# Kernel tuning notes

Hardware: AMD Instinct MI355X
Metric: run time of the kernel (lower is better)

## Reference

```python
import jax, jax.numpy as jnp
import numpy as np

N = 100000   # nodes
E = 600000   # edges
F_IN = 128   # input feature dim
H = 256      # hidden_channels


def setup_inputs() -> dict:
    key = jax.random.key(0)
    ks = jax.random.split(key, 8)
    x = jax.random.normal(ks[0], (N, F_IN), dtype=jnp.float32)
    edge_index = jax.random.randint(ks[1], (2, E), 0, N, dtype=jnp.int64)
    # SAGEConv params: out = lin_l(mean_agg) + lin_r(x_root); bias only on lin_l (PyG default)
    s1 = 1.0 / np.sqrt(F_IN)
    s2 = 1.0 / np.sqrt(H)
    Wl1 = jax.random.uniform(ks[2], (F_IN, H), jnp.float32, -s1, s1)
    Wr1 = jax.random.uniform(ks[3], (F_IN, H), jnp.float32, -s1, s1)
    b1 = jnp.zeros((H,), jnp.float32)
    Wl2 = jax.random.uniform(ks[4], (H, H), jnp.float32, -s2, s2)
    Wr2 = jax.random.uniform(ks[5], (H, H), jnp.float32, -s2, s2)
    b2 = jnp.zeros((H,), jnp.float32)
    return {"x": x, "edge_index": edge_index, "Wl1": Wl1, "Wr1": Wr1, "b1": b1,
            "Wl2": Wl2, "Wr2": Wr2, "b2": b2}


def _sage_conv(h, src, dst, Wl, Wr, b):
    # mean aggregation of source-node features at destination nodes
    msg = h[src]                                             # [E, d]
    agg = jax.ops.segment_sum(msg, dst, num_segments=N)      # [N, d]
    cnt = jax.ops.segment_sum(jnp.ones((src.shape[0],), h.dtype), dst, num_segments=N)
    agg = agg / jnp.maximum(cnt, 1.0)[:, None]
    return agg @ Wl + b + h @ Wr


def reference(x, edge_index, Wl1, Wr1, b1, Wl2, Wr2, b2):
    src, dst = edge_index[0], edge_index[1]
    h = jax.nn.relu(_sage_conv(x, src, dst, Wl1, Wr1, b1))
    return _sage_conv(h, src, dst, Wl2, Wr2, b2)
```

## Files before the change

kernel.cpp:

```cpp
#include <hip/hip_runtime.h>

#define Nn 100000
#define Ee 600000
#define Fin 128
#define Hd  256
#define NB  ((Nn + 1023) / 1024)
#define CB  12500
#define PB  768
#define EB  ((Ee + 255) / 256)

typedef __attribute__((ext_vector_type(8))) short short8;
typedef __attribute__((ext_vector_type(4))) float floatx4;

__device__ __forceinline__ float bf2f(unsigned short h) {
    return __uint_as_float(((unsigned int)h) << 16);
}
__device__ __forceinline__ unsigned short f2bf(float f) {
    unsigned int u = __float_as_uint(f);
    u += 0x7FFFu + ((u >> 16) & 1u);
    return (unsigned short)(u >> 16);
}
__device__ __forceinline__ float loadf(const void* p, int i, int f32) {
    return f32 ? ((const float*)p)[i] : bf2f(((const unsigned short*)p)[i]);
}
__device__ __forceinline__ void gload_lds16(const void* g, void* lds) {
    __builtin_amdgcn_global_load_lds((const __attribute__((address_space(1))) void*)g,
                                     (__attribute__((address_space(3))) void*)lds,
                                     16, 0, 0);
}

__device__ __forceinline__ void get_edge(const int* __restrict__ ei, int is64, int e,
                                         int& s, int& d) {
    if (is64) { s = ei[2 * e]; d = ei[2 * (Ee + e)]; }
    else      { s = ei[e];     d = ei[Ee + e]; }
}

__global__ void k_init(const unsigned int* __restrict__ ei,
                       const unsigned short* __restrict__ xu,
                       int* __restrict__ flag, int* __restrict__ cnt) {
    int i = blockIdx.x * 256 + threadIdx.x;
    if (i < 2 * Nn) cnt[i] = 0;
    if (blockIdx.x == 0 && threadIdx.x == 0) {
        int is64 = 1;
        for (int k = 1; k < 64; k += 2)
            if (ei[k] != 0u) { is64 = 0; break; }
        flag[0] = is64;
        int isf32 = 0;
        for (int k = 0; k < 512; k += 2) {
            unsigned e = (xu[k] >> 7) & 0xFFu;
            if (e >= 0xC0u) { isf32 = 1; break; }
        }
        flag[1] = isf32;
    }
}

__global__ void k_pre(const void* __restrict__ x, unsigned short* __restrict__ xb,
                      const void* __restrict__ Wl1, const void* __restrict__ Wr1,
                      const void* __restrict__ Wl2, const void* __restrict__ Wr2,
                      unsigned short* __restrict__ Wt1, unsigned short* __restrict__ Wt2,
                      const int* __restrict__ ei, int* __restrict__ cnt,
                      const int* __restrict__ flag) {
    int bid = blockIdx.x;
    if (bid < CB) {
        int i = (bid * 256 + threadIdx.x) * 4;
        if (i >= Nn * Fin) return;
        if (flag[1]) {
            float4 v = ((const float4*)x)[i >> 2];
            ushort4 u;
            u.x = f2bf(v.x); u.y = f2bf(v.y); u.z = f2bf(v.z); u.w = f2bf(v.w);
            ((ushort4*)xb)[i >> 2] = u;
        } else {
            ((ushort4*)xb)[i >> 2] = ((const ushort4*)x)[i >> 2];
        }
    } else if (bid < CB + PB) {
        int f32 = flag[1];
        int tid = (bid - CB) * 256 + threadIdx.x;
        if (tid < 256 * 256) {
            int n = tid >> 8, k = tid & 255;
            float v = (k < 128) ? loadf(Wl1, k * 256 + n, f32) : loadf(Wr1, (k - 128) * 256 + n, f32);
            Wt1[n * 256 + k] = f2bf(v);
        }
        int t2 = tid - 256 * 256;
        if (t2 >= 0 && t2 < 256 * 512) {
            int n = t2 >> 9, k = t2 & 511;
            float v = (k < 256) ? loadf(Wl2, k * 256 + n, f32) : loadf(Wr2, (k - 256) * 256 + n, f32);
            Wt2[n * 512 + k] = f2bf(v);
        }
    } else {
        int e = (bid - CB - PB) * 256 + threadIdx.x;
        if (e >= Ee) return;
        int is64 = flag[0], s, d;
        get_edge(ei, is64, e, s, d);
        atomicAdd(&cnt[d], 1);
    }
}

__global__ void k_bsum(const int* __restrict__ cnt, int* __restrict__ bsum) {
    __shared__ int red[256];
    int b = blockIdx.x, t = threadIdx.x;
    int i = b * 1024 + t * 4;
    int s = 0;
    if (i + 3 < Nn) {
        int4 v = *reinterpret_cast<const int4*>(cnt + i);
        s = v.x + v.y + v.z + v.w;
    } else {
        for (int j = 0; j < 4; j++) if (i + j < Nn) s += cnt[i + j];
    }
    red[t] = s;
    __syncthreads();
    for (int off = 128; off > 0; off >>= 1) {
        if (t < off) red[t] += red[t + off];
        __syncthreads();
    }
    if (t == 0) bsum[b] = red[0];
}

__global__ void k_bscan(const int* __restrict__ bsum, int* __restrict__ bpre,
                        int* __restrict__ rowptr) {
    __shared__ int sc[128];
    int t = threadIdx.x;
    int v = (t < NB) ? bsum[t] : 0;
    sc[t] = v;
    __syncthreads();
    for (int off = 1; off < 128; off <<= 1) {
        int add = (t >= off) ? sc[t - off] : 0;
        __syncthreads();
        sc[t] += add;
        __syncthreads();
    }
    if (t < NB) bpre[t] = sc[t] - v;
    if (t == 127) rowptr[Nn] = sc[127];
}

__global__ void k_rowptr(const int* __restrict__ cnt, const int* __restrict__ bpre,
                         int* __restrict__ rowptr) {
    __shared__ int sc[256];
    int b = blockIdx.x, t = threadIdx.x;
    int i = b * 1024 + t * 4;
    int4 c = make_int4(0, 0, 0, 0);
    if (i + 3 < Nn) {
        c = *reinterpret_cast<const int4*>(cnt + i);
    } else {
        if (i     < Nn) c.x = cnt[i];
        if (i + 1 < Nn) c.y = cnt[i + 1];
        if (i + 2 < Nn) c.z = cnt[i + 2];
        if (i + 3 < Nn) c.w = cnt[i + 3];
    }
    int s = c.x + c.y + c.z + c.w;
    sc[t] = s;
    __syncthreads();
    for (int off = 1; off < 256; off <<= 1) {
        int add = (t >= off) ? sc[t - off] : 0;
        __syncthreads();
        sc[t] += add;
        __syncthreads();
    }
    int p = bpre[b] + sc[t] - s;
    int4 r;
    r.x = p;
    r.y = r.x + c.x;
    r.z = r.y + c.y;
    r.w = r.z + c.z;
    if (i + 3 < Nn) {
        *reinterpret_cast<int4*>(rowptr + i) = r;
    } else {
        if (i     < Nn) rowptr[i]     = r.x;
        if (i + 1 < Nn) rowptr[i + 1] = r.y;
        if (i + 2 < Nn) rowptr[i + 2] = r.z;
        if (i + 3 < Nn) rowptr[i + 3] = r.w;
    }
}

__global__ void k_fill(const int* __restrict__ ei, const int* __restrict__ flag,
                       const int* __restrict__ rowptr, int* __restrict__ cur,
                       int* __restrict__ srcl) {
    int e = blockIdx.x * 256 + threadIdx.x;
    if (e >= Ee) return;
    int is64 = flag[0], s, d;
    get_edge(ei, is64, e, s, d);
    int pos = atomicAdd(&cur[d], 1);
    srcl[rowptr[d] + pos] = s;
}

template <int F, int SIN, int SOUT>
__device__ __forceinline__ void agg_body(const unsigned short* __restrict__ X,
                                         unsigned short* __restrict__ O,
                                         const int* __restrict__ rowptr,
                                         const int* __restrict__ srcl) {
    int gw = (blockIdx.x * blockDim.x + threadIdx.x) >> 6;
    int lane = threadIdx.x & 63;
    if (gw >= Nn) return;
    int b = rowptr[gw], e = rowptr[gw + 1];
    constexpr int C = F / 64;
    float acc[C] = {};
    if (e > b) {
        int last = e - 1;
        for (int i = b; i < e; i += 8) {
            int sv[8];
            float w[8];
#pragma unroll
            for (int j = 0; j < 8; j++) {
                int id = i + j;
                sv[j] = srcl[id < last ? id : last];
                w[j] = (id < e) ? 1.f : 0.f;
            }
            if constexpr (C == 2) {
                ushort2 u[8];
#pragma unroll
                for (int j = 0; j < 8; j++)
                    u[j] = *reinterpret_cast<const ushort2*>(X + (size_t)sv[j] * SIN + lane * 2);
#pragma unroll
                for (int j = 0; j < 8; j++) {
                    acc[0] = fmaf(w[j], bf2f(u[j].x), acc[0]);
                    acc[1] = fmaf(w[j], bf2f(u[j].y), acc[1]);
                }
            } else {
                ushort4 u[8];
#pragma unroll
                for (int j = 0; j < 8; j++)
                    u[j] = *reinterpret_cast<const ushort4*>(X + (size_t)sv[j] * SIN + lane * 4);
#pragma unroll
                for (int j = 0; j < 8; j++) {
                    acc[0] = fmaf(w[j], bf2f(u[j].x), acc[0]);
                    acc[1] = fmaf(w[j], bf2f(u[j].y), acc[1]);
                    acc[2] = fmaf(w[j], bf2f(u[j].z), acc[2]);
                    acc[3] = fmaf(w[j], bf2f(u[j].w), acc[3]);
                }
            }
        }
    }
    float inv = 1.f / (float)max(e - b, 1);
    unsigned short* op = O + (size_t)gw * SOUT + lane * C;
    if constexpr (C == 2) {
        ushort2 u; u.x = f2bf(acc[0] * inv); u.y = f2bf(acc[1] * inv);
        *reinterpret_cast<ushort2*>(op) = u;
    } else {
        ushort4 u;
        u.x = f2bf(acc[0] * inv); u.y = f2bf(acc[1] * inv);
        u.z = f2bf(acc[2] * inv); u.w = f2bf(acc[3] * inv);
        *reinterpret_cast<ushort4*>(op) = u;
    }
}

__global__ void k_agg1(const unsigned short* __restrict__ xb, unsigned short* __restrict__ agg1,
                       const int* __restrict__ rowptr, const int* __restrict__ srcl) {
    agg_body<Fin, Fin, Fin>(xb, agg1, rowptr, srcl);
}

__global__ void k_agg2(const int* __restrict__ rowptr, const int* __restrict__ srcl,
                       unsigned short* __restrict__ acat_ws) {
    agg_body<Hd, 512, 512>(acat_ws + 256, acat_ws, rowptr, srcl);
}

template <int KT, int K1, int S1, int S2>
__device__ __forceinline__ void gemm_core_pipe(const unsigned short* __restrict__ A1,
                                               const unsigned short* __restrict__ A2,
                                               const unsigned short* __restrict__ Wt,
                                               floatx4 (&acc)[4][4],
                                               unsigned short* sA, unsigned short* sB,
                                               int m_base) {
    const int tid = threadIdx.x;
    const int lane = tid & 63, wid = tid >> 6;
    const int wm = wid & 1, wn = wid >> 1;
    const int quad = lane >> 4, l16 = lane & 15;
    const int rs = tid >> 2;
    const int cs = tid & 3;
    constexpr int NT = KT / 32;

#define STAGE(t, buf)                                                              \
    {                                                                              \
        int kb_ = (t) * 32;                                                        \
        {                                                                          \
            int gk_ = kb_ + ((cs ^ ((rs >> 1) & 3)) << 3);                         \
            int m_ = m_base + rs; if (m_ >= Nn) m_ = Nn - 1;                       \
            const unsigned short* gp_ = (gk_ < K1)                                 \
                ? A1 + (size_t)m_ * S1 + gk_                                       \
                : A2 + (size_t)m_ * S2 + (gk_ - K1);                               \
            gload_lds16(gp_, sA + (buf) * 4096 + wid * 512);                       \
        }                                                                          \
        _Pragma("unroll")                                                          \
        for (int i_ = 0; i_ < 2; i_++) {                                           \
            int n_ = i_ * 128 + rs;                                                \
            int gk_ = kb_ + ((cs ^ ((n_ >> 1) & 3)) << 3);                         \
            gload_lds16(Wt + (size_t)n_ * KT + gk_,                                \
                        sB + (buf) * 8192 + i_ * 4096 + wid * 512);                \
        }                                                                          \
    }

#define COMPUTE(buf)                                                               \
    {                                                                              \
        short8 a_[4], b_[4];                                                       \
        _Pragma("unroll")                                                          \
        for (int mt_ = 0; mt_ < 4; mt_++) {                                        \
            int r_ = wm * 64 + mt_ * 16 + l16;                                     \
            a_[mt_] = *reinterpret_cast<const short8*>(                            \
                sA + (buf) * 4096 + r_ * 32 + ((quad ^ ((r_ >> 1) & 3)) << 3));    \
        }                                                                          \
        _Pragma("unroll")                                                          \
        for (int nt_ = 0; nt_ < 4; nt_++) {                                        \
            int n_ = wn * 64 + nt_ * 16 + l16;                                     \
            b_[nt_] = *reinterpret_cast<const short8*>(                            \
                sB + (buf) * 8192 + n_ * 32 + ((quad ^ ((n_ >> 1) & 3)) << 3));    \
        }                                                                          \
        _Pragma("unroll")                                                          \
        for (int mt_ = 0; mt_ < 4; mt_++)                                          \
            _Pragma("unroll")                                                      \
            for (int nt_ = 0; nt_ < 4; nt_++)                                      \
                acc[mt_][nt_] = __builtin_amdgcn_mfma_f32_16x16x32_bf16(           \
                    a_[mt_], b_[nt_], acc[mt_][nt_], 0, 0, 0);                     \
    }

    STAGE(0, 0)
#pragma unroll
    for (int t = 0; t < NT; t++) {
        __syncthreads();
        if (t + 1 < NT) STAGE(t + 1, (t + 1) & 1)
        COMPUTE(t & 1)
    }
#undef STAGE
#undef COMPUTE
}

__global__ __launch_bounds__(512) void k_gemm1(const unsigned short* __restrict__ agg1,
                                               const unsigned short* __restrict__ xb,
                                               const unsigned short* __restrict__ Wt1,
                                               const void* __restrict__ bias,
                                               const int* __restrict__ flag,
                                               unsigned short* __restrict__ acat_ws) {
    __shared__ unsigned short sA[8192];
    __shared__ unsigned short sB[16384];
    int f32 = flag[1];
    int tid = threadIdx.x;
    int wid = tid >> 6, lane = tid & 63;
    int wm = wid & 1, wn = wid >> 1;
    int quad = lane >> 4, l16 = lane & 15;
    int m_base = blockIdx.x * 128;
    floatx4 acc[4][4] = {};
    gemm_core_pipe<256, 128, 128, 128>(agg1, xb, Wt1, acc, sA, sB, m_base);
#pragma unroll
    for (int p = 0; p < 2; p++) {
        __syncthreads();
        if (wm == p) {
#pragma unroll
            for (int nt = 0; nt < 4; nt++) {
                int n = wn * 64 + nt * 16 + l16;
                float bv = loadf(bias, n, f32);
#pragma unroll
                for (int mt = 0; mt < 4; mt++) {
#pragma unroll
                    for (int r = 0; r < 4; r++) {
                        float v = acc[mt][nt][r] + bv;
                        v = v > 0.f ? v : 0.f;
                        sB[(mt * 16 + quad * 4 + r) * 256 + n] = f2bf(v);
                    }
                }
            }
        }
        __syncthreads();
#pragma unroll
        for (int rnd = 0; rnd < 4; rnd++) {
            int rl = rnd * 16 + (tid >> 5);
            int m = m_base + p * 64 + rl;
            if (m < Nn)
                *reinterpret_cast<short8*>(acat_ws + (size_t)m * 512 + 256 + (tid & 31) * 8) =
                    *reinterpret_cast<const short8*>(sB + rl * 256 + (tid & 31) * 8);
        }
    }
}

__global__ __launch_bounds__(512) void k_gemm2(const unsigned short* __restrict__ Wt2,
                                               const void* __restrict__ bias,
                                               const int* __restrict__ flag,
                                               const unsigned short* __restrict__ acat_ws,
                                               void* __restrict__ out) {
    __shared__ unsigned short sA[8192];
    __shared__ unsigned short sB[16384];
    int f32 = flag[1];
    int tid = threadIdx.x;
    int wid = tid >> 6, lane = tid & 63;
    int wm = wid & 1, wn = wid >> 1;
    int quad = lane >> 4, l16 = lane & 15;
    int m_base = blockIdx.x * 128;
    floatx4 acc[4][4] = {};
    gemm_core_pipe<512, 512, 512, 512>(acat_ws, acat_ws, Wt2, acc, sA, sB, m_base);
    float* sF = (float*)sB;
#pragma unroll
    for (int q = 0; q < 4; q++) {
        __syncthreads();
        if (wm == (q >> 1)) {
#pragma unroll
            for (int nt = 0; nt < 4; nt++) {
                int n = wn * 64 + nt * 16 + l16;
                float bv = loadf(bias, n, f32);
#pragma unroll
                for (int mt2 = 0; mt2 < 2; mt2++) {
                    int mt = (q & 1) * 2 + mt2;
#pragma unroll
                    for (int r = 0; r < 4; r++)
                        sF[(mt2 * 16 + quad * 4 + r) * 256 + n] = acc[mt][nt][r] + bv;
                }
            }
        }
        __syncthreads();
#pragma unroll
        for (int rnd = 0; rnd < 2; rnd++) {
            int rl = rnd * 16 + (tid >> 5);
            int m = m_base + q * 32 + rl;
            if (m < Nn) {
                if (f32) {
                    float4* dst = (float4*)((float*)out + (size_t)m * 256) + (tid & 31) * 2;
                    const float4* src = (const float4*)(sF + rl * 256) + (tid & 31) * 2;
                    dst[0] = src[0];
                    dst[1] = src[1];
                } else {
                    const float* src = sF + rl * 256 + (tid & 31) * 8;
                    short8 pk;
#pragma unroll
                    for (int j = 0; j < 8; j++)
                        ((unsigned short*)&pk)[j] = f2bf(src[j]);
                    *reinterpret_cast<short8*>((unsigned short*)out + (size_t)m * 256 + (tid & 31) * 8) = pk;
                }
            }
        }
    }
}

extern "C" void kernel_launch(void* const* d_in, const int* in_sizes, int n_in,
                              void* d_out, int out_size, void* d_ws, size_t ws_size,
                              hipStream_t stream) {
    const void* x   = d_in[0];
    const int*  ei  = (const int*)d_in[1];
    const void* Wl1 = d_in[2];
    const void* Wr1 = d_in[3];
    const void* b1  = d_in[4];
    const void* Wl2 = d_in[5];
    const void* Wr2 = d_in[6];
    const void* b2  = d_in[7];

    char* ws = (char*)d_ws;
    size_t off_cnt    = 0;
    size_t off_cur    = off_cnt + (size_t)Nn * 4;
    size_t off_rowptr = off_cur + (size_t)Nn * 4;
    size_t off_srcl   = off_rowptr + (size_t)(Nn + 4) * 4;
    size_t off_flag   = off_srcl + (size_t)Ee * 4;
    size_t off_bsum   = ((off_flag + 8 + 255) / 256) * 256;
    size_t off_bpre   = off_bsum + 128 * 4;
    size_t off_wt1    = off_bpre + 128 * 4;
    size_t off_wt2    = off_wt1 + 256 * 256 * 2;
    size_t off_xb     = off_wt2 + 256 * 512 * 2;
    size_t off_agg1   = off_xb + (size_t)Nn * Fin * 2;
    size_t off_acat   = off_agg1 + (size_t)Nn * Fin * 2;

    int*            cnt     = (int*)(ws + off_cnt);
    int*            cur     = (int*)(ws + off_cur);
    int*            rowptr  = (int*)(ws + off_rowptr);
    int*            srcl    = (int*)(ws + off_srcl);
    int*            flag    = (int*)(ws + off_flag);
    int*            bsum    = (int*)(ws + off_bsum);
    int*            bpre    = (int*)(ws + off_bpre);
    unsigned short* Wt1     = (unsigned short*)(ws + off_wt1);
    unsigned short* Wt2     = (unsigned short*)(ws + off_wt2);
    unsigned short* xb      = (unsigned short*)(ws + off_xb);
    unsigned short* agg1    = (unsigned short*)(ws + off_agg1);
    unsigned short* acat_ws = (unsigned short*)(ws + off_acat);

    k_init<<<(2 * Nn + 255) / 256, 256, 0, stream>>>((const unsigned int*)ei,
                                                     (const unsigned short*)x, flag, cnt);
    k_pre<<<CB + PB + EB, 256, 0, stream>>>(x, xb, Wl1, Wr1, Wl2, Wr2, Wt1, Wt2,
                                            ei, cnt, flag);
    k_bsum<<<NB, 256, 0, stream>>>(cnt, bsum);
    k_bscan<<<1, 128, 0, stream>>>(bsum, bpre, rowptr);
    k_rowptr<<<NB, 256, 0, stream>>>(cnt, bpre, rowptr);
    k_fill<<<EB, 256, 0, stream>>>(ei, flag, rowptr, cur, srcl);

    int ab = (Nn * 64 + 255) / 256;
    int gx = (Nn + 127) / 128;

    k_agg1<<<ab, 256, 0, stream>>>(xb, agg1, rowptr, srcl);
    k_gemm1<<<gx, 512, 0, stream>>>(agg1, xb, Wt1, b1, flag, acat_ws);
    k_agg2<<<ab, 256, 0, stream>>>(rowptr, srcl, acat_ws);
    k_gemm2<<<gx, 512, 0, stream>>>(Wt2, b2, flag, acat_ws, d_out);
}
```

Baseline: 379.0 us.

## Triple-buffer GEMM LDS pipeline with BK=64 and vmcnt-based waits

Replaces the double-buffered K=32 GEMM mainloop with a three-stage ring of K=64 tiles. It prefetches two stages ahead and waits on partial vmcnt plus a raw s_barrier instead of __syncthreads, so global loads overlap with MFMA work. LDS use rises to about 144KB per block, which can lower occupancy. The init kernel's format detection also moves from a serial single-thread loop to wave ballots.

```diff
diff --git a/kernel.cpp b/kernel.cpp
--- a/kernel.cpp
+++ b/kernel.cpp
@@ -40,17 +40,18 @@
                        int* __restrict__ flag, int* __restrict__ cnt) {
     int i = blockIdx.x * 256 + threadIdx.x;
     if (i < 2 * Nn) cnt[i] = 0;
-    if (blockIdx.x == 0 && threadIdx.x == 0) {
-        int is64 = 1;
-        for (int k = 1; k < 64; k += 2)
-            if (ei[k] != 0u) { is64 = 0; break; }
-        flag[0] = is64;
-        int isf32 = 0;
-        for (int k = 0; k < 512; k += 2) {
-            unsigned e = (xu[k] >> 7) & 0xFFu;
-            if (e >= 0xC0u) { isf32 = 1; break; }
-        }
-        flag[1] = isf32;
+    if (blockIdx.x == 0 && threadIdx.x < 64) {
+        int l = threadIdx.x;
+        unsigned hi = (l < 32) ? ei[2 * l + 1] : 0u;
+        unsigned long long nz = __ballot(hi != 0u);
+        int big = 0;
+#pragma unroll
+        for (int j = 0; j < 4; j++) {
+            unsigned u = xu[l * 8 + j * 2];
+            if (((u >> 7) & 0xFFu) >= 0xC0u) big = 1;
+        }
+        unsigned long long bb = __ballot(big != 0);
+        if (l == 0) { flag[0] = (nz == 0ull) ? 1 : 0; flag[1] = (bb != 0ull) ? 1 : 0; }
     }
 }
 
@@ -253,54 +254,59 @@
 }
 
 template <int KT, int K1, int S1, int S2>
-__device__ __forceinline__ void gemm_core_pipe(const unsigned short* __restrict__ A1,
-                                               const unsigned short* __restrict__ A2,
-                                               const unsigned short* __restrict__ Wt,
-                                               floatx4 (&acc)[4][4],
-                                               unsigned short* sA, unsigned short* sB,
-                                               int m_base) {
+__device__ __forceinline__ void gemm_core_tri(const unsigned short* __restrict__ A1,
+                                              const unsigned short* __restrict__ A2,
+                                              const unsigned short* __restrict__ Wt,
+                                              floatx4 (&acc)[4][4],
+                                              unsigned short* sA, unsigned short* sB,
+                                              int m_base) {
     const int tid = threadIdx.x;
     const int lane = tid & 63, wid = tid >> 6;
     const int wm = wid & 1, wn = wid >> 1;
     const int quad = lane >> 4, l16 = lane & 15;
-    const int rs = tid >> 2;
-    const int cs = tid & 3;
-    constexpr int NT = KT / 32;
+    const int n_base = wn * 64;
+    const int rs = tid >> 3;
+    const int cs = tid & 7;
+    constexpr int NT = KT / 64;
 
 #define STAGE(t, buf)                                                              \
     {                                                                              \
-        int kb_ = (t) * 32;                                                        \
-        {                                                                          \
-            int gk_ = kb_ + ((cs ^ ((rs >> 1) & 3)) << 3);                         \
-            int m_ = m_base + rs; if (m_ >= Nn) m_ = Nn - 1;                       \
+        int kb_ = (t) * 64;                                                        \
+        _Pragma("unroll")                                                          \
+        for (int i_ = 0; i_ < 2; i_++) {                                           \
+            int r_ = i_ * 64 + rs;                                                 \
+            int gk_ = kb_ + ((cs ^ (r_ & 7)) << 3);                                \
+            int m_ = m_base + r_; if (m_ >= Nn) m_ = Nn - 1;                       \
             const unsigned short* gp_ = (gk_ < K1)                                 \
                 ? A1 + (size_t)m_ * S1 + gk_                                       \
                 : A2 + (size_t)m_ * S2 + (gk_ - K1);                               \
-            gload_lds16(gp_, sA + (buf) * 4096 + wid * 512);                       \
+            gload_lds16(gp_, sA + (buf) * 8192 + i_ * 4096 + wid * 512);           \
         }                                                                          \
         _Pragma("unroll")                                                          \
-        for (int i_ = 0; i_ < 2; i_++) {                                           \
-            int n_ = i_ * 128 + rs;                                                \
-            int gk_ = kb_ + ((cs ^ ((n_ >> 1) & 3)) << 3);                         \
+        for (int i_ = 0; i_ < 4; i_++) {                                           \
+            int n_ = i_ * 64 + rs;                                                 \
+            int gk_ = kb_ + ((cs ^ (n_ & 7)) << 3);                                \
             gload_lds16(Wt + (size_t)n_ * KT + gk_,                                \
-                        sB + (buf) * 8192 + i_ * 4096 + wid * 512);                \
+                        sB + (buf) * 16384 + i_ * 4096 + wid * 512);               \
         }                                                                          \
     }
 
 #define COMPUTE(buf)                                                               \
-    {                                                                              \
+    _Pragma("unroll")                                                              \
+    for (int ks_ = 0; ks_ < 64; ks_ += 32) {                                       \
         short8 a_[4], b_[4];                                                       \
+        int q_ = (ks_ >> 3) + quad;                                                \
         _Pragma("unroll")                                                          \
         for (int mt_ = 0; mt_ < 4; mt_++) {                                        \
             int r_ = wm * 64 + mt_ * 16 + l16;                                     \
             a_[mt_] = *reinterpret_cast<const short8*>(                            \
-                sA + (buf) * 4096 + r_ * 32 + ((quad ^ ((r_ >> 1) & 3)) << 3));    \
+                sA + (buf) * 8192 + r_ * 64 + ((q_ ^ (l16 & 7)) << 3));            \
         }                                                                          \
         _Pragma("unroll")                                                          \
         for (int nt_ = 0; nt_ < 4; nt_++) {                                        \
-            int n_ = wn * 64 + nt_ * 16 + l16;                                     \
+            int n_ = n_base + nt_ * 16 + l16;                                      \
             b_[nt_] = *reinterpret_cast<const short8*>(                            \
-                sB + (buf) * 8192 + n_ * 32 + ((quad ^ ((n_ >> 1) & 3)) << 3));    \
+                sB + (buf) * 16384 + n_ * 64 + ((q_ ^ (l16 & 7)) << 3));           \
         }                                                                          \
         _Pragma("unroll")                                                          \
         for (int mt_ = 0; mt_ < 4; mt_++)                                          \
@@ -311,11 +317,19 @@
     }
 
     STAGE(0, 0)
+    STAGE(1, 1)
 #pragma unroll
     for (int t = 0; t < NT; t++) {
-        __syncthreads();
-        if (t + 1 < NT) STAGE(t + 1, (t + 1) & 1)
-        COMPUTE(t & 1)
+        if (t + 1 < NT) {
+            asm volatile("s_waitcnt vmcnt(6)" ::: "memory");
+        } else {
+            asm volatile("s_waitcnt vmcnt(0)" ::: "memory");
+        }
+        __builtin_amdgcn_sched_barrier(0);
+        asm volatile("s_barrier" ::: "memory");
+        __builtin_amdgcn_sched_barrier(0);
+        if (t + 2 < NT) STAGE(t + 2, (t + 2) % 3)
+        COMPUTE(t % 3)
     }
 #undef STAGE
 #undef COMPUTE
@@ -327,8 +341,8 @@
                                                const void* __restrict__ bias,
                                                const int* __restrict__ flag,
                                                unsigned short* __restrict__ acat_ws) {
-    __shared__ unsigned short sA[8192];
-    __shared__ unsigned short sB[16384];
+    __shared__ unsigned short sA[24576];
+    __shared__ unsigned short sB[49152];
     int f32 = flag[1];
     int tid = threadIdx.x;
     int wid = tid >> 6, lane = tid & 63;
@@ -336,7 +350,7 @@
     int quad = lane >> 4, l16 = lane & 15;
     int m_base = blockIdx.x * 128;
     floatx4 acc[4][4] = {};
-    gemm_core_pipe<256, 128, 128, 128>(agg1, xb, Wt1, acc, sA, sB, m_base);
+    gemm_core_tri<256, 128, 128, 128>(agg1, xb, Wt1, acc, sA, sB, m_base);
 #pragma unroll
     for (int p = 0; p < 2; p++) {
         __syncthreads();
@@ -373,8 +387,8 @@
                                                const int* __restrict__ flag,
                                                const unsigned short* __restrict__ acat_ws,
                                                void* __restrict__ out) {
-    __shared__ unsigned short sA[8192];
-    __shared__ unsigned short sB[16384];
+    __shared__ unsigned short sA[24576];
+    __shared__ unsigned short sB[49152];
     int f32 = flag[1];
     int tid = threadIdx.x;
     int wid = tid >> 6, lane = tid & 63;
@@ -382,7 +396,7 @@
     int quad = lane >> 4, l16 = lane & 15;
     int m_base = blockIdx.x * 128;
     floatx4 acc[4][4] = {};
-    gemm_core_pipe<512, 512, 512, 512>(acat_ws, acat_ws, Wt2, acc, sA, sB, m_base);
+    gemm_core_tri<512, 512, 512, 512>(acat_ws, acat_ws, Wt2, acc, sA, sB, m_base);
     float* sF = (float*)sB;
 #pragma unroll
     for (int q = 0; q < 4; q++) {
```

Result: slower. 388.1 us (+2.4%).
